# Performance work log

Measured on AMD Instinct MI355X. Metric: run time of the kernel, lower is better.

## Reference

```python
import jax, jax.numpy as jnp
import numpy as np
from jax import lax

DN = ('NCHW', 'OIHW', 'NCHW')

def conv(x, w, b, stride=1):
    y = lax.conv_general_dilated(x, w, window_strides=(stride, stride),
                                 padding='VALID', dimension_numbers=DN)
    return y + b[None, :, None, None]

def maxpool(x, k=3, s=2):
    return lax.reduce_window(x, -jnp.inf, lax.max,
                             (1, 1, k, k), (1, 1, s, s), 'VALID')

def setup_inputs() -> dict:
    key = jax.random.key(0)
    ks = jax.random.split(key, 7)
    B = 2048
    x = jax.random.normal(ks[0], (B, 1, 28, 28), dtype=jnp.float32)
    w1 = jax.random.normal(ks[1], (64, 1, 3, 3), dtype=jnp.float32)
    b1 = jax.random.normal(ks[2], (64,), dtype=jnp.float32)
    w2 = jax.random.normal(ks[3], (64, 64, 3, 3), dtype=jnp.float32)
    b2 = jax.random.normal(ks[4], (64,), dtype=jnp.float32)
    w3 = jax.random.normal(ks[5], (10, 64, 4, 4), dtype=jnp.float32)
    b3 = jax.random.normal(ks[6], (10,), dtype=jnp.float32)
    return {"x": x, "w1": w1, "b1": b1, "w2": w2, "b2": b2, "w3": w3, "b3": b3}

def reference(x, w1, b1, w2, b2, w3, b3):
    h = conv(x, w1, b1)            # [B,64,26,26]
    h = maxpool(h)                 # [B,64,12,12]
    h = jnp.maximum(h, 0.0)
    h = conv(h, w2, b2)            # [B,64,10,10]
    h = maxpool(h)                 # [B,64,4,4]
    h = jnp.maximum(h, 0.0)
    h = conv(h, w3, b3)            # [B,10,1,1]
    return h.reshape(h.shape[0], -1)  # [B,10]
```

## Files before the change

### kernel.cpp

```cpp
#include <hip/hip_runtime.h>


typedef __attribute__((ext_vector_type(8))) short short8;
typedef __attribute__((ext_vector_type(4))) float f32x4;

__device__ inline short f2bf(float f) {
    union { float f; unsigned u; } v; v.f = f;
    unsigned r = (v.u + 0x7FFFu + ((v.u >> 16) & 1u)) >> 16;
    return (short)r;
}

__global__ __launch_bounds__(256) void prep_w2(const float* __restrict__ w2,
                                               short* __restrict__ w2r) {
    int i = blockIdx.x * 256 + threadIdx.x;
    if (i >= 36864) return;
    int s = i >> 12, cout = (i >> 6) & 63, cin = i & 63;
    w2r[i] = f2bf(w2[cout * 576 + cin * 9 + s]);
}

__global__ __launch_bounds__(256) void convnet_fused(
    const float* __restrict__ x,
    const float* __restrict__ w1,
    const float* __restrict__ b1,
    const short* __restrict__ w2r,
    const float* __restrict__ b2,
    const float* __restrict__ w3,
    const float* __restrict__ b3,
    float* __restrict__ out)
{
    __shared__ float lds_f[7424];
    short* h1t  = (short*)lds_f;
    float* img  = lds_f + 5184;
    float* cbuf = lds_f;
    float* h2t  = lds_f + 6400;
    float* prt  = lds_f;

    const int n_img = blockIdx.x;
    const int t = threadIdx.x;
    const int c = t >> 2;
    const int q = t & 3;

    const float* img_g = x + (size_t)n_img * 784;
    for (int i = t; i < 784; i += 256) img[i] = img_g[i];
    __syncthreads();

    {
        const int oy = (q >> 1) * 6, ox = (q & 1) * 6;
        const int iy0 = 2 * oy, ix0 = 2 * ox;
        float w[9];
        #pragma unroll
        for (int k = 0; k < 9; ++k) w[k] = w1[c * 9 + k];
        const float bias = b1[c];

        float in0[15], in1[15], in2[15];
        #pragma unroll
        for (int s = 0; s < 15; ++s) in0[s] = img[(iy0 + 0) * 28 + ix0 + s];
        #pragma unroll
        for (int s = 0; s < 15; ++s) in1[s] = img[(iy0 + 1) * 28 + ix0 + s];
        float cm[3][6];

        #pragma unroll
        for (int r = 0; r < 13; ++r) {
            #pragma unroll
            for (int s = 0; s < 15; ++s) in2[s] = img[(iy0 + r + 2) * 28 + ix0 + s];
            #pragma unroll
            for (int px = 0; px < 6; ++px) cm[r % 3][px] = -1e30f;
            #pragma unroll
            for (int xx = 0; xx < 13; ++xx) {
                float a = bias;
                #pragma unroll
                for (int j = 0; j < 3; ++j) {
                    a += in0[xx + j] * w[j];
                    a += in1[xx + j] * w[3 + j];
                    a += in2[xx + j] * w[6 + j];
                }
                if ((xx & 1) == 0) {
                    if (xx >= 2 && xx <= 12) cm[r % 3][xx / 2 - 1] = fmaxf(cm[r % 3][xx / 2 - 1], a);
                    if (xx <= 10)            cm[r % 3][xx / 2]     = fmaxf(cm[r % 3][xx / 2], a);
                } else {
                    cm[r % 3][xx / 2] = fmaxf(cm[r % 3][xx / 2], a);
                }
            }
            if (r >= 2 && (r & 1) == 0) {
                const int py = r / 2 - 1;
                #pragma unroll
                for (int px = 0; px < 6; ++px) {
                    float m = fmaxf(fmaxf(cm[0][px], cm[1][px]), cm[2][px]);
                    h1t[((oy + py) * 12 + ox + px) * 72 + c] = f2bf(fmaxf(m, 0.0f));
                }
            }
            #pragma unroll
            for (int s = 0; s < 15; ++s) { in0[s] = in1[s]; in1[s] = in2[s]; }
        }
    }
    __syncthreads();

    const int wv = t >> 6, lane = t & 63;
    const int quad = lane >> 4, mrow = lane & 15;
    {
        int base_el[7];
        #pragma unroll
        for (int nt = 0; nt < 7; ++nt) {
            int n = nt * 16 + mrow; if (n > 99) n = 99;
            int y = n / 10, xx = n - y * 10;
            base_el[nt] = (y * 12 + xx) * 72;
        }
        f32x4 acc[7];
        #pragma unroll
        for (int nt = 0; nt < 7; ++nt) acc[nt] = (f32x4){0.f, 0.f, 0.f, 0.f};

        #pragma unroll
        for (int ks = 0; ks < 18; ++ks) {
            const int s = ks >> 1, h = ks & 1;
            const int ky = s / 3, kx = s - ky * 3;
            const short8 a = *(const short8*)(w2r + s * 4096 + (wv * 16 + mrow) * 64
                                              + h * 32 + quad * 8);
            #pragma unroll
            for (int nt = 0; nt < 7; ++nt) {
                const short8 b = *(const short8*)(h1t + base_el[nt]
                                                  + (ky * 12 + kx) * 72 + h * 32 + quad * 8);
                acc[nt] = __builtin_amdgcn_mfma_f32_16x16x32_bf16(a, b, acc[nt], 0, 0, 0);
            }
        }
        __syncthreads();
        #pragma unroll
        for (int nt = 0; nt < 7; ++nt) {
            const int n = nt * 16 + mrow;
            if (n < 100) {
                #pragma unroll
                for (int r = 0; r < 4; ++r) {
                    const int cout = wv * 16 + quad * 4 + r;
                    cbuf[cout * 100 + n] = acc[nt][r] + b2[cout];
                }
            }
        }
    }
    __syncthreads();

    {
        const float* cb = cbuf + c * 100;
        #pragma unroll
        for (int k = 0; k < 4; ++k) {
            const int pos = q * 4 + k;
            const int py = pos >> 2, px = pos & 3;
            float m = -1e30f;
            #pragma unroll
            for (int a = 0; a < 3; ++a)
                #pragma unroll
                for (int b = 0; b < 3; ++b)
                    m = fmaxf(m, cb[(2 * py + a) * 10 + (2 * px + b)]);
            h2t[pos * 64 + c] = fmaxf(m, 0.0f);
        }
    }
    __syncthreads();

    if (t < 160) {
        const int o = t >> 4, l = t & 15;
        const float* w3o = w3 + o * 1024;
        float s = 0.0f;
        #pragma unroll
        for (int cc = 0; cc < 4; ++cc) {
            const int cin = l * 4 + cc;
            const float4 wv4a = *(const float4*)(w3o + cin * 16);
            const float4 wv4b = *(const float4*)(w3o + cin * 16 + 4);
            const float4 wv4c = *(const float4*)(w3o + cin * 16 + 8);
            const float4 wv4d = *(const float4*)(w3o + cin * 16 + 12);
            const float* hh = h2t + cin;
            s += hh[0*64] * wv4a.x + hh[1*64] * wv4a.y + hh[2*64] * wv4a.z + hh[3*64] * wv4a.w;
            s += hh[4*64] * wv4b.x + hh[5*64] * wv4b.y + hh[6*64] * wv4b.z + hh[7*64] * wv4b.w;
            s += hh[8*64] * wv4c.x + hh[9*64] * wv4c.y + hh[10*64] * wv4c.z + hh[11*64] * wv4c.w;
            s += hh[12*64] * wv4d.x + hh[13*64] * wv4d.y + hh[14*64] * wv4d.z + hh[15*64] * wv4d.w;
        }
        prt[t] = s;
    }
    __syncthreads();
    if (t < 10) {
        float s = b3[t];
        #pragma unroll
        for (int l = 0; l < 16; ++l) s += prt[t * 16 + l];
        out[(size_t)n_img * 10 + t] = s;
    }
}

extern "C" void kernel_launch(void* const* d_in, const int* in_sizes, int n_in,
                              void* d_out, int out_size, void* d_ws, size_t ws_size,
                              hipStream_t stream) {
    const float* x  = (const float*)d_in[0];
    const float* w1 = (const float*)d_in[1];
    const float* b1 = (const float*)d_in[2];
    const float* w2 = (const float*)d_in[3];
    const float* b2 = (const float*)d_in[4];
    const float* w3 = (const float*)d_in[5];
    const float* b3 = (const float*)d_in[6];
    float* out = (float*)d_out;
    short* w2r = (short*)d_ws;

    const int B = in_sizes[0] / 784;
    prep_w2<<<144, 256, 0, stream>>>(w2, w2r);
    convnet_fused<<<B, 256, 0, stream>>>(x, w1, b1, w2r, b2, w3, b3, out);
}
```

Measured before the change: 109.1 us.

## Split fused convnet into conv1+pool kernel and conv2+rest kernel via global buffer

Splits the single fused kernel into two kernels: conv1+maxpool writes bf16 activations to a global workspace buffer, then a second kernel runs the conv2 MFMA, pool and conv3 by reading B operands directly from global memory. The aim is to shrink LDS use and drop the image staging and the extra syncs, so occupancy goes up. In exchange it adds a global round trip of about 37 MB for the intermediate activations and a second launch. It also stores the conv2 output as bf16 in LDS with padded strides, which adds a rounding step that the fp32 version did not have. The old fused path is kept as a fallback when the workspace is too small.

```diff
diff --git a/kernel.cpp b/kernel.cpp
--- a/kernel.cpp
+++ b/kernel.cpp
@@ -8,6 +8,10 @@
     union { float f; unsigned u; } v; v.f = f;
     unsigned r = (v.u + 0x7FFFu + ((v.u >> 16) & 1u)) >> 16;
     return (short)r;
+}
+__device__ inline float bf2f(short s) {
+    union { unsigned u; float f; } v; v.u = ((unsigned)(unsigned short)s) << 16;
+    return v.f;
 }
 
 __global__ __launch_bounds__(256) void prep_w2(const float* __restrict__ w2,
@@ -18,15 +22,184 @@
     w2r[i] = f2bf(w2[cout * 576 + cin * 9 + s]);
 }
 
-__global__ __launch_bounds__(256) void convnet_fused(
+#define EL(arr, s) ((s & 3) == 0 ? arr[(s) >> 2].x : \
+                    (s & 3) == 1 ? arr[(s) >> 2].y : \
+                    (s & 3) == 2 ? arr[(s) >> 2].z : arr[(s) >> 2].w)
+
+__global__ __launch_bounds__(256) void conv1_pool(
     const float* __restrict__ x,
     const float* __restrict__ w1,
     const float* __restrict__ b1,
+    short* __restrict__ h1g)
+{
+    const int n_img = blockIdx.x;
+    const int t = threadIdx.x;
+    const int c = t & 63;
+    const int q = t >> 6;
+    const int oy = (q >> 1) * 6, ox = (q & 1) * 6;
+    const int iy0 = 2 * oy, ix0 = 2 * ox;
+    const float* img = x + (size_t)n_img * 784;
+    short* h1o = h1g + (size_t)n_img * 9216;
+
+    float w[9];
+    #pragma unroll
+    for (int k = 0; k < 9; ++k) w[k] = w1[c * 9 + k];
+    const float bias = b1[c];
+
+    float4 in0[4], in1[4], in2[4];
+    #define LOADROW4(dst, row) do { \
+        const float4* p4 = (const float4*)(img + (row) * 28 + ix0); \
+        dst[0] = p4[0]; dst[1] = p4[1]; dst[2] = p4[2]; dst[3] = p4[3]; } while (0)
+
+    LOADROW4(in0, iy0 + 0);
+    LOADROW4(in1, iy0 + 1);
+    float cm[3][6];
+
+    #pragma unroll
+    for (int r = 0; r < 13; ++r) {
+        LOADROW4(in2, iy0 + r + 2);
+        #pragma unroll
+        for (int px = 0; px < 6; ++px) cm[r % 3][px] = -1e30f;
+        #pragma unroll
+        for (int xx = 0; xx < 13; ++xx) {
+            float a = bias;
+            #pragma unroll
+            for (int j = 0; j < 3; ++j) {
+                a += EL(in0, xx + j) * w[j];
+                a += EL(in1, xx + j) * w[3 + j];
+                a += EL(in2, xx + j) * w[6 + j];
+            }
+            if ((xx & 1) == 0) {
+                if (xx >= 2 && xx <= 12) cm[r % 3][xx / 2 - 1] = fmaxf(cm[r % 3][xx / 2 - 1], a);
+                if (xx <= 10)            cm[r % 3][xx / 2]     = fmaxf(cm[r % 3][xx / 2], a);
+            } else {
+                cm[r % 3][xx / 2] = fmaxf(cm[r % 3][xx / 2], a);
+            }
+        }
+        if (r >= 2 && (r & 1) == 0) {
+            const int py = r / 2 - 1;
+            #pragma unroll
+            for (int px = 0; px < 6; ++px) {
+                float m = fmaxf(fmaxf(cm[0][px], cm[1][px]), cm[2][px]);
+                h1o[((oy + py) * 12 + ox + px) * 64 + c] = f2bf(fmaxf(m, 0.0f));
+            }
+        }
+        #pragma unroll
+        for (int i = 0; i < 4; ++i) { in0[i] = in1[i]; in1[i] = in2[i]; }
+    }
+    #undef LOADROW4
+}
+
+__global__ __launch_bounds__(256) void conv2_rest(
+    const short* __restrict__ h1g,
     const short* __restrict__ w2r,
     const float* __restrict__ b2,
     const float* __restrict__ w3,
     const float* __restrict__ b3,
     float* __restrict__ out)
+{
+    __shared__ float lds_f[4272];
+    short* cbuf = (short*)lds_f;
+    float* h2t  = lds_f + 3232;
+    float* prt  = lds_f;
+
+    const int n_img = blockIdx.x;
+    const int t = threadIdx.x;
+    const int c = t >> 2;
+    const int q = t & 3;
+    const int wv = t >> 6, lane = t & 63;
+    const int quad = lane >> 4, mrow = lane & 15;
+    const short* h1 = h1g + (size_t)n_img * 9216;
+
+    {
+        int pos_b[7];
+        #pragma unroll
+        for (int nt = 0; nt < 7; ++nt) {
+            int n = nt * 16 + mrow; if (n > 99) n = 99;
+            int y = n / 10, xx = n - y * 10;
+            pos_b[nt] = y * 12 + xx;
+        }
+        f32x4 acc[7];
+        #pragma unroll
+        for (int nt = 0; nt < 7; ++nt) acc[nt] = (f32x4){0.f, 0.f, 0.f, 0.f};
+
+        #pragma unroll
+        for (int ks = 0; ks < 18; ++ks) {
+            const int s = ks >> 1, h = ks & 1;
+            const int ky = s / 3, kx = s - ky * 3;
+            const int koff = ky * 12 + kx;
+            const int hoff = h * 32 + quad * 8;
+            const short8 a = *(const short8*)(w2r + s * 4096 + (wv * 16 + mrow) * 64 + hoff);
+            #pragma unroll
+            for (int nt = 0; nt < 7; ++nt) {
+                const short8 b = *(const short8*)(h1 + (pos_b[nt] + koff) * 64 + hoff);
+                acc[nt] = __builtin_amdgcn_mfma_f32_16x16x32_bf16(a, b, acc[nt], 0, 0, 0);
+            }
+        }
+        #pragma unroll
+        for (int nt = 0; nt < 7; ++nt) {
+            const int n = nt * 16 + mrow;
+            if (n < 100) {
+                #pragma unroll
+                for (int r = 0; r < 4; ++r) {
+                    const int cout = wv * 16 + quad * 4 + r;
+                    cbuf[cout * 101 + n] = f2bf(acc[nt][r] + b2[cout]);
+                }
+            }
+        }
+    }
+    __syncthreads();
+
+    {
+        const short* cb = cbuf + c * 101;
+        #pragma unroll
+        for (int k = 0; k < 4; ++k) {
+            const int pos = q * 4 + k;
+            const int py = pos >> 2, px = pos & 3;
+            float m = -1e30f;
+            #pragma unroll
+            for (int a = 0; a < 3; ++a)
+                #pragma unroll
+                for (int b = 0; b < 3; ++b)
+                    m = fmaxf(m, bf2f(cb[(2 * py + a) * 10 + (2 * px + b)]));
+            h2t[pos * 65 + c] = fmaxf(m, 0.0f);
+        }
+    }
+    __syncthreads();
+
+    if (t < 160) {
+        const int o = t >> 4, l = t & 15;
+        const float* w3o = w3 + o * 1024;
+        float s = 0.0f;
+        #pragma unroll
+        for (int cc = 0; cc < 4; ++cc) {
+            const int cin = l * 4 + cc;
+            const float4 wv4a = *(const float4*)(w3o + cin * 16);
+            const float4 wv4b = *(const float4*)(w3o + cin * 16 + 4);
+            const float4 wv4c = *(const float4*)(w3o + cin * 16 + 8);
+            const float4 wv4d = *(const float4*)(w3o + cin * 16 + 12);
+            const float* hh = h2t + cin;
+            s += hh[0*65] * wv4a.x + hh[1*65] * wv4a.y + hh[2*65] * wv4a.z + hh[3*65] * wv4a.w;
+            s += hh[4*65] * wv4b.x + hh[5*65] * wv4b.y + hh[6*65] * wv4b.z + hh[7*65] * wv4b.w;
+            s += hh[8*65] * wv4c.x + hh[9*65] * wv4c.y + hh[10*65] * wv4c.z + hh[11*65] * wv4c.w;
+            s += hh[12*65] * wv4d.x + hh[13*65] * wv4d.y + hh[14*65] * wv4d.z + hh[15*65] * wv4d.w;
+        }
+        prt[t] = s;
+    }
+    __syncthreads();
+    if (t < 10) {
+        float s = b3[t];
+        #pragma unroll
+        for (int l = 0; l < 16; ++l) s += prt[t * 16 + l];
+        out[(size_t)n_img * 10 + t] = s;
+    }
+}
+
+__global__ __launch_bounds__(256) void convnet_fused(
+    const float* __restrict__ x, const float* __restrict__ w1,
+    const float* __restrict__ b1, const short* __restrict__ w2r,
+    const float* __restrict__ b2, const float* __restrict__ w3,
+    const float* __restrict__ b3, float* __restrict__ out)
 {
     __shared__ float lds_f[7424];
     short* h1t  = (short*)lds_f;
@@ -51,14 +224,12 @@
         #pragma unroll
         for (int k = 0; k < 9; ++k) w[k] = w1[c * 9 + k];
         const float bias = b1[c];
-
         float in0[15], in1[15], in2[15];
         #pragma unroll
         for (int s = 0; s < 15; ++s) in0[s] = img[(iy0 + 0) * 28 + ix0 + s];
         #pragma unroll
         for (int s = 0; s < 15; ++s) in1[s] = img[(iy0 + 1) * 28 + ix0 + s];
         float cm[3][6];
-
         #pragma unroll
         for (int r = 0; r < 13; ++r) {
             #pragma unroll
@@ -108,7 +279,6 @@
         f32x4 acc[7];
         #pragma unroll
         for (int nt = 0; nt < 7; ++nt) acc[nt] = (f32x4){0.f, 0.f, 0.f, 0.f};
-
         #pragma unroll
         for (int ks = 0; ks < 18; ++ks) {
             const int s = ks >> 1, h = ks & 1;
@@ -136,7 +306,6 @@
         }
     }
     __syncthreads();
-
     {
         const float* cb = cbuf + c * 100;
         #pragma unroll
@@ -153,7 +322,6 @@
         }
     }
     __syncthreads();
-
     if (t < 160) {
         const int o = t >> 4, l = t & 15;
         const float* w3o = w3 + o * 1024;
@@ -196,6 +364,14 @@
     short* w2r = (short*)d_ws;
 
     const int B = in_sizes[0] / 784;
+    const size_t need = 73728u + (size_t)B * 9216u * 2u;
+
     prep_w2<<<144, 256, 0, stream>>>(w2, w2r);
-    convnet_fused<<<B, 256, 0, stream>>>(x, w1, b1, w2r, b2, w3, b3, out);
-}
+    if (ws_size >= need) {
+        short* h1g = (short*)((char*)d_ws + 73728);
+        conv1_pool<<<B, 256, 0, stream>>>(x, w1, b1, h1g);
+        conv2_rest<<<B, 256, 0, stream>>>(h1g, w2r, b2, w3, b3, out);
+    } else {
+        convnet_fused<<<B, 256, 0, stream>>>(x, w1, b1, w2r, b2, w3, b3, out);
+    }
+}
```

Measured after the change: 223.3 us. +104.8%, slower.
